# Optimization experiments

Hardware: AMD Instinct MI355X
Metric: run time of the kernel (lower is better)

Reference implementation:

```python
import jax, jax.numpy as jnp
import numpy as np

N = 20000      # nodes per graph
E = 640000     # edges per graph
FIN = 256      # input feature dim
H = 512        # hidden dim
K = 1000       # top_k


def _ln(x, g, b):
    m = jnp.mean(x, axis=-1, keepdims=True)
    v = jnp.var(x, axis=-1, keepdims=True)
    return (x - m) / jnp.sqrt(v + 1e-5) * g + b


def _gin_conv(x, src, dst, w1, b1, w2, b2):
    # GINConv with eps=0: mlp(x + sum_{j->i} x_j)
    agg = jax.ops.segment_sum(x[src], dst, num_segments=N)
    h = x + agg
    return jax.nn.relu(h @ w1 + b1) @ w2 + b2


def _gnn(x, edge_index, layers, lin_w, lin_b):
    src, dst = edge_index[0], edge_index[1]
    for (w1, b1, w2, b2) in layers:
        x = jax.nn.relu(_gin_conv(x, src, dst, w1, b1, w2, b2))
    return x @ lin_w + lin_b  # [N, 2]


def setup_inputs() -> dict:
    key = jax.random.key(0)
    ks = iter(jax.random.split(key, 40))
    w = lambda shape, s=0.02: jax.random.normal(next(ks), shape, jnp.float32) * s
    d = {}
    d["x1"] = jax.random.normal(next(ks), (N, FIN), jnp.float32)
    d["edge_index1"] = jax.random.randint(next(ks), (2, E), 0, N)
    d["x2"] = jax.random.normal(next(ks), (N, FIN), jnp.float32)
    d["edge_index2"] = jax.random.randint(next(ks), (2, E), 0, N)
    d["g_w11"] = w((FIN, H)); d["g_b11"] = jnp.zeros((H,), jnp.float32)
    d["g_w12"] = w((H, H));   d["g_b12"] = jnp.zeros((H,), jnp.float32)
    d["g_w21"] = w((H, H));   d["g_b21"] = jnp.zeros((H,), jnp.float32)
    d["g_w22"] = w((H, H));   d["g_b22"] = jnp.zeros((H,), jnp.float32)
    d["g_w31"] = w((H, H));   d["g_b31"] = jnp.zeros((H,), jnp.float32)
    d["g_w32"] = w((H, H));   d["g_b32"] = jnp.zeros((H,), jnp.float32)
    d["lin_w"] = w((H, 2));   d["lin_b"] = jnp.zeros((2,), jnp.float32)
    d["fc1_w"] = w((K, 128)); d["fc1_b"] = jnp.zeros((128,), jnp.float32)
    d["ln1_g"] = jnp.ones((128,), jnp.float32); d["ln1_b"] = jnp.zeros((128,), jnp.float32)
    d["fc2_w"] = w((128, H)); d["fc2_b"] = jnp.zeros((H,), jnp.float32)
    d["ln2_g"] = jnp.ones((H,), jnp.float32); d["ln2_b"] = jnp.zeros((H,), jnp.float32)
    d["fc3_w"] = w((H, 1));   d["fc3_b"] = jnp.zeros((1,), jnp.float32)
    return d


def reference(x1, edge_index1, x2, edge_index2,
              g_w11, g_b11, g_w12, g_b12,
              g_w21, g_b21, g_w22, g_b22,
              g_w31, g_b31, g_w32, g_b32,
              lin_w, lin_b,
              fc1_w, fc1_b, ln1_g, ln1_b,
              fc2_w, fc2_b, ln2_g, ln2_b,
              fc3_w, fc3_b):
    layers = [(g_w11, g_b11, g_w12, g_b12),
              (g_w21, g_b21, g_w22, g_b22),
              (g_w31, g_b31, g_w32, g_b32)]
    o1 = _gnn(x1, edge_index1, layers, lin_w, lin_b)  # [N, 2]
    o2 = _gnn(x2, edge_index2, layers, lin_w, lin_b)  # [N, 2]
    # torch.nn.PairwiseDistance(p=2, eps=1e-6): ||x1 - x2 + eps||_2 per row
    dist = jnp.sqrt(jnp.sum((o1 - o2 + 1e-6) ** 2, axis=-1))  # [N]
    vals, _ = jax.lax.top_k(dist, K)  # descending, matches torch.topk
    h = vals @ fc1_w + fc1_b
    h = jax.nn.relu(_ln(h, ln1_g, ln1_b))
    # dropout is identity in eval mode
    h = h @ fc2_w + fc2_b
    h = jax.nn.relu(_ln(h, ln2_g, ln2_b))
    return jax.nn.sigmoid(h @ fc3_w + fc3_b)  # [1]
```

## Files before the change

kernel.cpp:

```cpp
#include <hip/hip_runtime.h>
#include <hip/hip_bf16.h>
#include <math.h>

#define N1      20000
#define NT      40000
#define E1      640000
#define ET      1280000
#define FIN_D   256
#define HID_D   512
#define TOPK    1000
#define MP1     20096
#define NGEMM   628
#define AGG256  1250
#define AGG512  2500

#define NB       157
#define CAP      10240
#define BK_CHUNK 8192

typedef __attribute__((ext_vector_type(8))) short short8;
typedef __attribute__((ext_vector_type(4))) float floatx4;
typedef __attribute__((ext_vector_type(2))) float floatx2;
typedef unsigned int uintx4 __attribute__((ext_vector_type(4)));

__device__ __forceinline__ unsigned short f2bf(float f) {
    union { __hip_bfloat16 h; unsigned short u; } cv;
    cv.h = __float2bfloat16(f);
    return cv.u;
}
__device__ __forceinline__ float bflo(unsigned int u) {
    union { unsigned int i; float f; } c; c.i = u << 16; return c.f;
}
__device__ __forceinline__ float bfhi(unsigned int u) {
    union { unsigned int i; float f; } c; c.i = u & 0xffff0000u; return c.f;
}

__device__ __forceinline__ void gmap(int b, int& bx, int& by) {
    const int nfull = (157 / 8) * 32;
    if (b < nfull) {
        int chunk = b >> 5, w = b & 31;
        bx = (chunk << 3) + (w & 7);
        by = w >> 3;
    } else {
        int i = b - nfull;
        bx = 152 + i % 5;
        by = i / 5;
    }
}

__device__ __forceinline__ void convw_body(int bl, int K, float* tile ,
                                           const float* __restrict__ W,
                                           unsigned short* __restrict__ Wt) {
    int kb = K / 32;
    int k0 = (bl % kb) * 32, n0 = (bl / kb) * 32;
    int tx = threadIdx.x & 31, ty = threadIdx.x >> 5;
    for (int r = ty; r < 32; r += 8) tile[r * 33 + tx] = W[(size_t)(k0 + r) * HID_D + n0 + tx];
    __syncthreads();
    for (int r = ty; r < 32; r += 8)
        Wt[(size_t)(n0 + r) * K + k0 + tx] = f2bf(tile[tx * 33 + r]);
}
__device__ __forceinline__ void convx_body(int i, const float* __restrict__ x,
                                           unsigned char* __restrict__ x8) {
    float4 f = ((const float4*)x)[i];
    int p = __builtin_amdgcn_cvt_pk_fp8_f32(f.x, f.y, 0, false);
    p = __builtin_amdgcn_cvt_pk_fp8_f32(f.z, f.w, p, true);
    ((unsigned int*)x8)[i] = (unsigned int)p;
}

__device__ __forceinline__ void bucketA_body(int bb, int t,
                                             const int* __restrict__ ei1,
                                             const int* __restrict__ ei2,
                                             unsigned int* __restrict__ stageG,
                                             int* __restrict__ gcnt,
                                             unsigned int* shb) {
    unsigned int* stg   = shb;
    unsigned int* scn   = shb + 8192;
    unsigned int* hoff  = shb + 8448;
    unsigned int* hcur  = shb + 8608;
    unsigned int* hbase = shb + 8768;
    int e0 = bb * BK_CHUNK;
    int total = ET - e0; if (total > BK_CHUNK) total = BK_CHUNK;
    for (int i = t; i < 160; i += 256) hcur[i] = 0;
    __syncthreads();
    for (int k = 0; k < 32; ++k) {
        int e = e0 + k * 256 + t;
        if (e < ET) {
            int d = (e < E1) ? ei1[E1 + e] : (ei2[E1 + (e - E1)] + N1);
            atomicAdd(&hcur[d >> 8], 1u);
        }
    }
    __syncthreads();
    unsigned int v = (t < NB) ? hcur[t] : 0u;
    scn[t] = v; __syncthreads();
    for (int off = 1; off < 256; off <<= 1) {
        unsigned int x = (t >= off) ? scn[t - off] : 0u;
        __syncthreads(); scn[t] += x; __syncthreads();
    }
    if (t < NB) {
        unsigned int ex = scn[t] - v;
        hoff[t] = ex;
        hbase[t] = (unsigned int)atomicAdd(&gcnt[t], (int)v);
    }
    __syncthreads();
    if (t < NB) hcur[t] = hoff[t];
    __syncthreads();
    for (int k = 0; k < 32; ++k) {
        int e = e0 + k * 256 + t;
        if (e < ET) {
            int s, d;
            if (e < E1) { s = ei1[e]; d = ei1[E1 + e]; }
            else        { int ee = e - E1; s = ei2[ee] + N1; d = ei2[E1 + ee] + N1; }
            unsigned int b8 = (unsigned int)(d >> 8);
            unsigned int pos = atomicAdd(&hcur[b8], 1u);
            stg[pos] = (unsigned int)s | ((unsigned int)(d & 255) << 16) | (b8 << 24);
        }
    }
    __syncthreads();
    for (int i = t; i < total; i += 256) {
        unsigned int e = stg[i];
        unsigned int b8 = e >> 24;
        unsigned int g = hbase[b8] + ((unsigned int)i - hoff[b8]);
        if (g < CAP) stageG[(size_t)b8 * CAP + g] = e;
    }
}

__device__ __forceinline__ void sort_body(int b, int t,
                                          const unsigned int* __restrict__ stageG,
                                          const int* __restrict__ gcnt,
                                          int* __restrict__ row_start,
                                          unsigned short* __restrict__ csr,
                                          unsigned int* shb) {
    unsigned int* cnts = shb;
    unsigned int* offs = shb + 256;
    unsigned int* cur  = shb + 512;
    unsigned int* scn  = shb + 768;
    unsigned short* outb = (unsigned short*)(shb + 1024);
    int* s_base = (int*)(shb + 6144);
    unsigned int gv = (t < NB) ? (unsigned int)gcnt[t] : 0u;
    scn[t] = gv; __syncthreads();
    for (int off = 1; off < 256; off <<= 1) {
        unsigned int x = (t >= off) ? scn[t - off] : 0u;
        __syncthreads(); scn[t] += x; __syncthreads();
    }
    if (t == b) s_base[0] = (int)(scn[t] - gv);
    cnts[t] = 0;
    __syncthreads();
    int base = s_base[0];
    int cnt = gcnt[b]; if (cnt > CAP) cnt = CAP;
    const unsigned int* src = stageG + (size_t)b * CAP;
    for (int i = t; i < cnt; i += 256) atomicAdd(&cnts[(src[i] >> 16) & 255], 1u);
    __syncthreads();
    unsigned int v = cnts[t];
    offs[t] = v; __syncthreads();
    for (int off = 1; off < 256; off <<= 1) {
        unsigned int x = (t >= off) ? offs[t - off] : 0u;
        __syncthreads(); offs[t] += x; __syncthreads();
    }
    unsigned int excl = offs[t] - v;
    cur[t] = excl;
    int node = b * 256 + t;
    if (node < NT) row_start[node] = base + (int)excl;
    if (b == 0 && t == 0) row_start[NT] = ET;
    __syncthreads();
    for (int i = t; i < cnt; i += 256) {
        unsigned int e = src[i];
        unsigned int p = atomicAdd(&cur[(e >> 16) & 255], 1u);
        outb[p] = (unsigned short)(e & 0xffffu);
    }
    __syncthreads();
    for (int i = t; i < cnt; i += 256) csr[base + i] = outb[i];
}

#define ACC4(u) do { \
    acc2[0] += __builtin_amdgcn_cvt_pk_f32_fp8((int)(u).x, false); \
    acc2[1] += __builtin_amdgcn_cvt_pk_f32_fp8((int)(u).x, true);  \
    acc2[2] += __builtin_amdgcn_cvt_pk_f32_fp8((int)(u).y, false); \
    acc2[3] += __builtin_amdgcn_cvt_pk_f32_fp8((int)(u).y, true);  \
    acc2[4] += __builtin_amdgcn_cvt_pk_f32_fp8((int)(u).z, false); \
    acc2[5] += __builtin_amdgcn_cvt_pk_f32_fp8((int)(u).z, true);  \
    acc2[6] += __builtin_amdgcn_cvt_pk_f32_fp8((int)(u).w, false); \
    acc2[7] += __builtin_amdgcn_cvt_pk_f32_fp8((int)(u).w, true);  } while (0)

template<int LPR4, int NSLAB>
__device__ __forceinline__ void agg8_body(int ab, int tid,
                                          const unsigned char* __restrict__ x8,
                                          const int* __restrict__ row_start,
                                          const unsigned short* __restrict__ csr,
                                          unsigned short* __restrict__ h, int n0) {
    int slab = ab & (NSLAB - 1);
    int grp  = ab / NSLAB;
    int node = grp * 32 + (tid >> 3);
    int lanec = tid & 7;
    int chunk = slab * 8 + lanec;
    const uint4* Xc = (const uint4*)x8 + chunk;
    floatx2 acc2[8] = {};
    uint4 v = Xc[(size_t)node * LPR4];
    ACC4(v);
    int nid = n0 + node;
    int s = row_start[nid], e = row_start[nid + 1];
    int p = s;
    int nb = (e - s) >> 3;
    uint4 a0, a1, a2, a3, a4, a5, a6, a7;
    uint4 b0, b1, b2, b3, b4, b5, b6, b7;
#define LOAD8(R, P) do { \
    int q0 = (int)csr[(P) + 0] - n0, q1 = (int)csr[(P) + 1] - n0; \
    int q2 = (int)csr[(P) + 2] - n0, q3 = (int)csr[(P) + 3] - n0; \
    int q4 = (int)csr[(P) + 4] - n0, q5 = (int)csr[(P) + 5] - n0; \
    int q6 = (int)csr[(P) + 6] - n0, q7 = (int)csr[(P) + 7] - n0; \
    R##0 = Xc[(size_t)q0 * LPR4]; R##1 = Xc[(size_t)q1 * LPR4]; \
    R##2 = Xc[(size_t)q2 * LPR4]; R##3 = Xc[(size_t)q3 * LPR4]; \
    R##4 = Xc[(size_t)q4 * LPR4]; R##5 = Xc[(size_t)q5 * LPR4]; \
    R##6 = Xc[(size_t)q6 * LPR4]; R##7 = Xc[(size_t)q7 * LPR4]; } while (0)
#define ACC8(R) do { ACC4(R##0); ACC4(R##1); ACC4(R##2); ACC4(R##3); \
                     ACC4(R##4); ACC4(R##5); ACC4(R##6); ACC4(R##7); } while (0)
    if (nb > 0) {
        LOAD8(a, p); p += 8;
        int i = 1;
        for (; i + 1 < nb; i += 2) {
            LOAD8(b, p); p += 8;
            ACC8(a);
            LOAD8(a, p); p += 8;
            ACC8(b);
        }
        if (i < nb) { LOAD8(b, p); p += 8; ACC8(a); ACC8(b); }
        else        { ACC8(a); }
    }
#undef LOAD8
#undef ACC8
    for (; p + 2 <= e; p += 2) {
        int ma = (int)csr[p + 0] - n0, mb = (int)csr[p + 1] - n0;
        uint4 u0 = Xc[(size_t)ma * LPR4];
        uint4 u1 = Xc[(size_t)mb * LPR4];
        ACC4(u0); ACC4(u1);
    }
    if (p < e) {
        int ma = (int)csr[p] - n0;
        uint4 u0 = Xc[(size_t)ma * LPR4];
        ACC4(u0);
    }
    unsigned int ow[8];
#pragma unroll
    for (int i = 0; i < 8; ++i)
        ow[i] = (unsigned)f2bf(acc2[i].x) | ((unsigned)f2bf(acc2[i].y) << 16);
    uintx4 o0, o1;
    o0.x = ow[0]; o0.y = ow[1]; o0.z = ow[2]; o0.w = ow[3];
    o1.x = ow[4]; o1.y = ow[5]; o1.z = ow[6]; o1.w = ow[7];
    size_t base = ((size_t)node * LPR4 + chunk) * 2;
    ((uintx4*)h)[base + 0] = o0;
    ((uintx4*)h)[base + 1] = o1;
}

__launch_bounds__(256)
__global__ void prep1_kernel(const int* __restrict__ ei1, const int* __restrict__ ei2,
                             unsigned int* __restrict__ stageG, int* __restrict__ gcnt,
                             const float* __restrict__ x1, unsigned char* __restrict__ x8) {
    __shared__ unsigned int shb[8928];
    int b = blockIdx.x;
    if (b < NB) bucketA_body(b, threadIdx.x, ei1, ei2, stageG, gcnt, shb);
    else convx_body((b - NB) * 256 + threadIdx.x, x1, x8);
}

__launch_bounds__(256)
__global__ void fused_sortx(const unsigned int* __restrict__ stageG,
                            const int* __restrict__ gcnt,
                            int* __restrict__ row_start,
                            unsigned short* __restrict__ csr,
                            const float* __restrict__ x2,
                            unsigned char* __restrict__ x8g2) {
    __shared__ unsigned int shb[6152];
    int b = blockIdx.x;
    if (b < NB) sort_body(b, threadIdx.x, stageG, gcnt, row_start, csr, shb);
    else convx_body((b - NB) * 256 + threadIdx.x, x2, x8g2);
}

__launch_bounds__(256, 4)
__global__ void fused_aggw(const unsigned char* __restrict__ x8,
                           const int* __restrict__ row_start,
                           const unsigned short* __restrict__ csr,
                           unsigned short* __restrict__ h,
                           const float* w11, unsigned short* wt11,
                           const float* w12, unsigned short* wt12,
                           const float* w21, unsigned short* wt21,
                           const float* w22, unsigned short* wt22,
                           const float* w31, unsigned short* wt31,
                           const float* w32, unsigned short* wt32) {
    __shared__ float tile[32 * 33];
    int b = blockIdx.x;
    if (b < AGG256) {
        agg8_body<16, 2>(b, threadIdx.x, x8, row_start, csr, h, 0);
    } else {
        int bl = b - AGG256;
        if (bl < 128)       convw_body(bl,        FIN_D, tile, w11, wt11);
        else if (bl < 384)  convw_body(bl - 128,  HID_D, tile, w12, wt12);
        else if (bl < 640)  convw_body(bl - 384,  HID_D, tile, w21, wt21);
        else if (bl < 896)  convw_body(bl - 640,  HID_D, tile, w22, wt22);
        else if (bl < 1152) convw_body(bl - 896,  HID_D, tile, w31, wt31);
        else                convw_body(bl - 1152, HID_D, tile, w32, wt32);
    }
}

__device__ __forceinline__ void store_fp8_tile(int row0, int col0, int tid,
                                               unsigned short* smem,
                                               floatx4 acc[4][4], const float* __restrict__ bias,
                                               unsigned char* __restrict__ C8,
                                               int wr, int wc, int lane) {
    unsigned char* tile = (unsigned char*)smem;
    int q = lane >> 4, cn = lane & 15;
#pragma unroll
    for (int j = 0; j < 4; ++j) {
        int lcol = wc * 64 + j * 16 + cn;
        float bv = bias[col0 + lcol];
#pragma unroll
        for (int i = 0; i < 4; ++i) {
            int lrow = wr * 64 + i * 16 + q * 4;
#pragma unroll
            for (int r = 0; r < 4; ++r) {
                float vv = fmaxf(acc[i][j][r] + bv, 0.f);
                int t8 = __builtin_amdgcn_cvt_pk_fp8_f32(vv, 0.f, 0, false);
                tile[(lrow + r) * 128 + lcol] = (unsigned char)(t8 & 0xff);
            }
        }
    }
    __syncthreads();
#pragma unroll
    for (int it = 0; it < 4; ++it) {
        int idx = it * 256 + tid;
        int lrow = idx >> 3, c16 = idx & 7;
        *(uint4*)(C8 + (size_t)(row0 + lrow) * HID_D + col0 + c16 * 16) =
            *(const uint4*)(tile + lrow * 128 + c16 * 16);
    }
}

__device__ __forceinline__ void gemm_body_db(int bx, int by, int tid,
                                             unsigned short* smem,
                                             const unsigned short* __restrict__ A,
                                             const unsigned short* __restrict__ Wt,
                                             const float* __restrict__ bias,
                                             unsigned short* __restrict__ C,
                                             unsigned char* __restrict__ C8, int K) {
    const int N = HID_D;
    int lane = tid & 63;
    int w = tid >> 6;
    int wr = w >> 1, wc = w & 1;
    int row0 = bx * 128;
    int col0 = by * 128;
    floatx4 acc[4][4] = {};
    int lr = tid >> 2;
    int c8 = (tid & 3) * 8;
    const unsigned short* Ag = A + (size_t)row0 * K;
    const unsigned short* Bg = Wt + (size_t)col0 * K;
    int nt = K >> 5;
    {
        unsigned short* As = smem;
        unsigned short* Bs = smem + 4096;
#pragma unroll
        for (int l = 0; l < 2; ++l) {
            int r = l * 64 + lr;
            __builtin_amdgcn_global_load_lds(
                (const __attribute__((address_space(1))) void*)(Ag + (size_t)r * K + c8),
                (__attribute__((address_space(3))) void*)(As + l * 2048 + tid * 8),
                16, 0, 0);
            __builtin_amdgcn_global_load_lds(
                (const __attribute__((address_space(1))) void*)(Bg + (size_t)r * K + c8),
                (__attribute__((address_space(3))) void*)(Bs + l * 2048 + tid * 8),
                16, 0, 0);
        }
    }
    __syncthreads();
    for (int t = 0; t < nt; ++t) {
        unsigned short* As = smem + ((t & 1) ? 8192 : 0);
        unsigned short* Bs = As + 4096;
        if (t + 1 < nt) {
            unsigned short* An = smem + ((t & 1) ? 0 : 8192);
            unsigned short* Bn = An + 4096;
            int kt = (t + 1) << 5;
#pragma unroll
            for (int l = 0; l < 2; ++l) {
                int r = l * 64 + lr;
                __builtin_amdgcn_global_load_lds(
                    (const __attribute__((address_space(1))) void*)(Ag + (size_t)r * K + kt + c8),
                    (__attribute__((address_space(3))) void*)(An + l * 2048 + tid * 8),
                    16, 0, 0);
                __builtin_amdgcn_global_load_lds(
                    (const __attribute__((address_space(1))) void*)(Bg + (size_t)r * K + kt + c8),
                    (__attribute__((address_space(3))) void*)(Bn + l * 2048 + tid * 8),
                    16, 0, 0);
            }
        }
        short8 af[4], bf[4];
        int q8 = (lane >> 4) * 8;
#pragma unroll
        for (int i = 0; i < 4; ++i) {
            int m = wr * 64 + i * 16 + (lane & 15);
            af[i] = *(const short8*)&As[m * 32 + q8];
            int n = wc * 64 + i * 16 + (lane & 15);
            bf[i] = *(const short8*)&Bs[n * 32 + q8];
        }
#pragma unroll
        for (int i = 0; i < 4; ++i)
#pragma unroll
            for (int j = 0; j < 4; ++j)
                acc[i][j] = __builtin_amdgcn_mfma_f32_16x16x32_bf16(af[i], bf[j], acc[i][j], 0, 0, 0);
        __syncthreads();
    }
    if (C8) {
        store_fp8_tile(row0, col0, tid, smem, acc, bias, C8, wr, wc, lane);
        return;
    }
    int q = lane >> 4;
    int cn = lane & 15;
#pragma unroll
    for (int j = 0; j < 4; ++j) {
        int col = col0 + wc * 64 + j * 16 + cn;
        float bv = bias[col];
#pragma unroll
        for (int i = 0; i < 4; ++i) {
            int rowb = row0 + wr * 64 + i * 16 + q * 4;
#pragma unroll
            for (int r = 0; r < 4; ++r) {
                float vv = fmaxf(acc[i][j][r] + bv, 0.f);
                C[(size_t)(rowb + r) * N + col] = f2bf(vv);
            }
        }
    }
}

__launch_bounds__(256)
__global__ void gemm_pair(const unsigned short* __restrict__ A1,
                          const unsigned short* __restrict__ W1,
                          const float* __restrict__ b1,
                          unsigned short* __restrict__ C1, unsigned char* C81, int K1,
                          const unsigned short* __restrict__ A2,
                          const unsigned short* __restrict__ W2,
                          const float* __restrict__ b2,
                          unsigned short* __restrict__ C2, unsigned char* C82, int K2) {
    __shared__ unsigned short smem[16384];
    int b = blockIdx.x;
    int bx, by;
    if (b < NGEMM) {
        gmap(b, bx, by);
        gemm_body_db(bx, by, threadIdx.x, smem, A1, W1, b1, C1, C81, K1);
    } else {
        gmap(b - NGEMM, bx, by);
        gemm_body_db(bx, by, threadIdx.x, smem, A2, W2, b2, C2, C82, K2);
    }
}

template<int LPR4, int NSLAB>
__launch_bounds__(256)
__global__ void fused_k(const unsigned short* __restrict__ A,
                        const unsigned short* __restrict__ Wt,
                        const float* __restrict__ bias,
                        unsigned short* __restrict__ C, unsigned char* C8, int K,
                        const unsigned char* __restrict__ x8,
                        const int* __restrict__ row_start,
                        const unsigned short* __restrict__ csr,
                        unsigned short* __restrict__ h, int n0, int nGemm) {
    __shared__ unsigned short smem[16384];
    int b = blockIdx.x;
    if (b < nGemm) {
        int bx, by;
        gmap(b, bx, by);
        gemm_body_db(bx, by, threadIdx.x, smem, A, Wt, bias, C, C8, K);
    } else {
        agg8_body<LPR4, NSLAB>(b - nGemm, threadIdx.x, x8, row_start, csr, h, n0);
    }
}

__device__ __forceinline__ void lin_body(int bb, int tid, const unsigned short* __restrict__ A,
                                         const float* __restrict__ w, const float* __restrict__ b,
                                         float* __restrict__ o, int M) {
    int wave = tid >> 6;
    int lane = tid & 63;
    int row = bb * 4 + wave;
    if (row >= M) return;
    const uint4* Ar = (const uint4*)(A + (size_t)row * 512);
    uint4 u = Ar[lane];
    float f[8];
    f[0] = bflo(u.x); f[1] = bfhi(u.x); f[2] = bflo(u.y); f[3] = bfhi(u.y);
    f[4] = bflo(u.z); f[5] = bfhi(u.z); f[6] = bflo(u.w); f[7] = bfhi(u.w);
    float s0 = 0.f, s1 = 0.f;
#pragma unroll
    for (int j = 0; j < 8; ++j) {
        int base = (lane * 8 + j) * 2;
        s0 = fmaf(f[j], w[base + 0], s0);
        s1 = fmaf(f[j], w[base + 1], s1);
    }
#pragma unroll
    for (int off = 32; off > 0; off >>= 1) {
        s0 += __shfl_down(s0, off, 64);
        s1 += __shfl_down(s1, off, 64);
    }
    if (lane == 0) { o[row * 2] = s0 + b[0]; o[row * 2 + 1] = s1 + b[1]; }
}

__launch_bounds__(256)
__global__ void fused_gemmlin(const unsigned short* __restrict__ A,
                              const unsigned short* __restrict__ Wt,
                              const float* __restrict__ bias,
                              unsigned short* __restrict__ C, int K,
                              const unsigned short* __restrict__ L,
                              const float* __restrict__ lw, const float* __restrict__ lb,
                              float* __restrict__ o) {
    __shared__ unsigned short smem[16384];
    int b = blockIdx.x;
    if (b < NGEMM) {
        int bx, by;
        gmap(b, bx, by);
        gemm_body_db(bx, by, threadIdx.x, smem, A, Wt, bias, C, nullptr, K);
    } else {
        lin_body(b - NGEMM, threadIdx.x, L, lw, lb, o, N1);
    }
}

__global__ void lin_dist_kernel(const unsigned short* __restrict__ A,
                                const float* __restrict__ w, const float* __restrict__ b,
                                const float* __restrict__ o1,
                                float* __restrict__ o2out,
                                float* __restrict__ dist) {
    int tid = threadIdx.x;
    int wave = tid >> 6;
    int lane = tid & 63;
    int row = blockIdx.x * 4 + wave;
    if (row >= N1) return;
    const uint4* Ar = (const uint4*)(A + (size_t)row * 512);
    uint4 u = Ar[lane];
    float f[8];
    f[0] = bflo(u.x); f[1] = bfhi(u.x); f[2] = bflo(u.y); f[3] = bfhi(u.y);
    f[4] = bflo(u.z); f[5] = bfhi(u.z); f[6] = bflo(u.w); f[7] = bfhi(u.w);
    float s0 = 0.f, s1 = 0.f;
#pragma unroll
    for (int j = 0; j < 8; ++j) {
        int base = (lane * 8 + j) * 2;
        s0 = fmaf(f[j], w[base + 0], s0);
        s1 = fmaf(f[j], w[base + 1], s1);
    }
#pragma unroll
    for (int off = 32; off > 0; off >>= 1) {
        s0 += __shfl_down(s0, off, 64);
        s1 += __shfl_down(s1, off, 64);
    }
    if (lane == 0) {
        float vx = s0 + b[0], vy = s1 + b[1];
        o2out[row * 2] = vx; o2out[row * 2 + 1] = vy;
        float2 a = ((const float2*)o1)[row];
        float d0 = a.x - vx + 1e-6f, d1 = a.y - vy + 1e-6f;
        dist[row] = sqrtf(d0 * d0 + d1 * d1);
    }
}

#define HBLK 20
#define HPB  1000
__launch_bounds__(256)
__global__ void hist_lds_kernel(const float* __restrict__ dist, int* __restrict__ hist) {
    __shared__ int lh[4096];
    int t = threadIdx.x;
    for (int i = t; i < 4096; i += 256) lh[i] = 0;
    __syncthreads();
    int base = blockIdx.x * HPB;
    for (int i = t; i < HPB; i += 256) {
        int idx = base + i;
        if (idx < N1) atomicAdd(&lh[__float_as_uint(dist[idx]) >> 19], 1);
    }
    __syncthreads();
    for (int i = t; i < 4096; i += 256) {
        int v = lh[i];
        if (v) atomicAdd(&hist[i], v);
    }
}

__global__ void selk_kernel(const int* __restrict__ hist, int* __restrict__ selout) {
    __shared__ int tile[256];
    int t = threadIdx.x;
    int running = 0;
    for (int tb = 0; tb < 16; ++tb) {
        int idx = 4095 - (tb * 256 + t);
        int v = hist[idx];
        tile[t] = v;
        __syncthreads();
        for (int off = 1; off < 256; off <<= 1) {
            int x = (t >= off) ? tile[t - off] : 0;
            __syncthreads();
            tile[t] += x;
            __syncthreads();
        }
        int incl = running + tile[t];
        if (incl >= TOPK && incl - v < TOPK) selout[0] = idx;
        running += tile[255];
        __syncthreads();
        if (running >= TOPK) break;
    }
}

__global__ void compact_kernel(const float* __restrict__ dist, const int* __restrict__ selout,
                               int* __restrict__ nc, float* __restrict__ cd, int* __restrict__ ci) {
    int i = blockIdx.x * blockDim.x + threadIdx.x;
    if (i >= N1) return;
    float d = dist[i];
    int b = (int)(__float_as_uint(d) >> 19);
    if (b >= selout[0]) {
        int p = atomicAdd(nc, 1);
        cd[p] = d;
        ci[p] = i;
    }
}

#define CCH 2048
__global__ void rankc_kernel(const float* __restrict__ cd, const int* __restrict__ ci,
                             const int* __restrict__ nc_p, float* __restrict__ vals) {
    __shared__ float ds[CCH];
    __shared__ int   di_[CCH];
    int nc = *nc_p;
    if (blockIdx.x * 256 >= nc) return;
    int t = threadIdx.x;
    int q = blockIdx.x * 256 + t;
    float dq = 0.f; int iq = 0;
    if (q < nc) { dq = cd[q]; iq = ci[q]; }
    int cnt = 0;
    for (int c0 = 0; c0 < nc; c0 += CCH) {
        int lim = min(CCH, nc - c0);
        for (int j = t; j < lim; j += 256) { ds[j] = cd[c0 + j]; di_[j] = ci[c0 + j]; }
        __syncthreads();
        if (q < nc) {
            for (int j = 0; j < lim; ++j) {
                float dj = ds[j];
                cnt += (dj > dq) || (dj == dq && di_[j] < iq);
            }
        }
        __syncthreads();
    }
    if (q < nc && cnt < TOPK) vals[cnt] = dq;
}

__launch_bounds__(512)
__global__ void head_kernel(const float* __restrict__ vals,
                            const float* __restrict__ fc1_w, const float* __restrict__ fc1_b,
                            const float* __restrict__ ln1_g, const float* __restrict__ ln1_b,
                            const float* __restrict__ fc2_w, const float* __restrict__ fc2_b,
                            const float* __restrict__ ln2_g, const float* __restrict__ ln2_b,
                            const float* __restrict__ fc3_w, const float* __restrict__ fc3_b,
                            float* __restrict__ out) {
    __shared__ float sv[TOPK];
    __shared__ float a1[128];
    __shared__ float red[512];
    __shared__ float s_m, s_r;
    int t = threadIdx.x;
    for (int i = t; i < TOPK; i += 512) sv[i] = vals[i];
    __syncthreads();
    int g = t >> 7, c = t & 127;
    float part = 0.f;
    for (int j = g * 250; j < g * 250 + 250; ++j)
        part = fmaf(sv[j], fc1_w[j * 128 + c], part);
    red[t] = part;
    __syncthreads();
    float h1 = 0.f;
    if (t < 128) h1 = fc1_b[t] + red[t] + red[t + 128] + red[t + 256] + red[t + 384];
    __syncthreads();
    red[t] = (t < 128) ? h1 : 0.f; __syncthreads();
    for (int s = 256; s > 0; s >>= 1) { if (t < s) red[t] += red[t + s]; __syncthreads(); }
    if (t == 0) s_m = red[0] / 128.f;
    __syncthreads();
    float m1 = s_m;
    float dv = (t < 128) ? (h1 - m1) : 0.f;
    red[t] = dv * dv; __syncthreads();
    for (int s = 256; s > 0; s >>= 1) { if (t < s) red[t] += red[t + s]; __syncthreads(); }
    if (t == 0) s_r = rsqrtf(red[0] / 128.f + 1e-5f);
    __syncthreads();
    float r1 = s_r;
    if (t < 128) a1[t] = fmaxf((h1 - m1) * r1 * ln1_g[t] + ln1_b[t], 0.f);
    __syncthreads();
    float h2 = fc2_b[t];
    for (int j = 0; j < 128; ++j) h2 = fmaf(a1[j], fc2_w[j * 512 + t], h2);
    red[t] = h2; __syncthreads();
    for (int s = 256; s > 0; s >>= 1) { if (t < s) red[t] += red[t + s]; __syncthreads(); }
    if (t == 0) s_m = red[0] / 512.f;
    __syncthreads();
    float m2 = s_m;
    float d2 = h2 - m2;
    red[t] = d2 * d2; __syncthreads();
    for (int s = 256; s > 0; s >>= 1) { if (t < s) red[t] += red[t + s]; __syncthreads(); }
    if (t == 0) s_r = rsqrtf(red[0] / 512.f + 1e-5f);
    __syncthreads();
    float r2 = s_r;
    float y2 = fmaxf((h2 - m2) * r2 * ln2_g[t] + ln2_b[t], 0.f);
    red[t] = y2 * fc3_w[t]; __syncthreads();
    for (int s = 256; s > 0; s >>= 1) { if (t < s) red[t] += red[t + s]; __syncthreads(); }
    if (t == 0) out[0] = 1.f / (1.f + expf(-(red[0] + fc3_b[0])));
}

extern "C" void kernel_launch(void* const* d_in, const int* in_sizes, int n_in,
                              void* d_out, int out_size, void* d_ws, size_t ws_size,
                              hipStream_t stream) {
    const float* x1   = (const float*)d_in[0];
    const int*   ei1  = (const int*)d_in[1];
    const float* x2   = (const float*)d_in[2];
    const int*   ei2  = (const int*)d_in[3];
    const float* w11  = (const float*)d_in[4];
    const float* b11  = (const float*)d_in[5];
    const float* w12  = (const float*)d_in[6];
    const float* b12  = (const float*)d_in[7];
    const float* w21  = (const float*)d_in[8];
    const float* b21  = (const float*)d_in[9];
    const float* w22  = (const float*)d_in[10];
    const float* b22  = (const float*)d_in[11];
    const float* w31  = (const float*)d_in[12];
    const float* b31  = (const float*)d_in[13];
    const float* w32  = (const float*)d_in[14];
    const float* b32  = (const float*)d_in[15];
    const float* lw   = (const float*)d_in[16];
    const float* lb   = (const float*)d_in[17];
    const float* fc1w = (const float*)d_in[18];
    const float* fc1b = (const float*)d_in[19];
    const float* ln1g = (const float*)d_in[20];
    const float* ln1b = (const float*)d_in[21];
    const float* fc2w = (const float*)d_in[22];
    const float* fc2b = (const float*)d_in[23];
    const float* ln2g = (const float*)d_in[24];
    const float* ln2b = (const float*)d_in[25];
    const float* fc3w = (const float*)d_in[26];
    const float* fc3b = (const float*)d_in[27];

    char* ws = (char*)d_ws;
    size_t off = 0;
    auto alloc = [&](size_t bytes) -> void* {
        void* p = ws + off;
        off += (bytes + 255) & ~(size_t)255;
        return p;
    };
    unsigned char*  XB8 = (unsigned char*)alloc((size_t)NT * FIN_D);
    unsigned short* H0a = (unsigned short*)alloc((size_t)MP1 * HID_D * 2);
    unsigned short* H1a = (unsigned short*)alloc((size_t)MP1 * HID_D * 2);
    unsigned short* H0b = (unsigned short*)alloc((size_t)MP1 * HID_D * 2);
    unsigned short* H1b = (unsigned short*)alloc((size_t)MP1 * HID_D * 2);
    unsigned char*  F8a = (unsigned char*)alloc((size_t)MP1 * HID_D);
    unsigned char*  F8b = (unsigned char*)alloc((size_t)MP1 * HID_D);
    unsigned short* wt11 = (unsigned short*)alloc((size_t)HID_D * FIN_D * 2);
    unsigned short* wt12 = (unsigned short*)alloc((size_t)HID_D * HID_D * 2);
    unsigned short* wt21 = (unsigned short*)alloc((size_t)HID_D * HID_D * 2);
    unsigned short* wt22 = (unsigned short*)alloc((size_t)HID_D * HID_D * 2);
    unsigned short* wt31 = (unsigned short*)alloc((size_t)HID_D * HID_D * 2);
    unsigned short* wt32 = (unsigned short*)alloc((size_t)HID_D * HID_D * 2);
    float* o         = (float*)alloc((size_t)NT * 2 * 4);
    float* dist      = (float*)alloc((size_t)N1 * 4);
    float* vals      = (float*)alloc((size_t)TOPK * 4);
    int*   row_start = (int*)alloc((size_t)(NT + 1) * 4);
    unsigned short* csr16 = (unsigned short*)alloc((size_t)ET * 2);
    unsigned int* stageG  = (unsigned int*)alloc((size_t)NB * CAP * 4);
    int*   gcnt      = (int*)alloc((size_t)160 * 4);
    int*   selblk    = (int*)alloc((size_t)(4096 + 64) * 4);
    int*   hist      = selblk;
    int*   nc        = selblk + 4096;
    int*   selout    = (int*)alloc(2 * 4);
    float* cd        = (float*)alloc((size_t)N1 * 4);
    int*   ci        = (int*)alloc((size_t)N1 * 4);

    const unsigned char* XB8g2 = XB8 + (size_t)N1 * FIN_D;

    hipMemsetAsync(gcnt, 0, 160 * sizeof(int), stream);
    hipMemsetAsync(selblk, 0, (4096 + 64) * sizeof(int), stream);
    prep1_kernel<<<NB + 5000, 256, 0, stream>>>(ei1, ei2, stageG, gcnt, x1, XB8);
    fused_sortx<<<NB + 5000, 256, 0, stream>>>(stageG, gcnt, row_start, csr16,
                                               x2, (unsigned char*)XB8g2);
    fused_aggw<<<AGG256 + 1408, 256, 0, stream>>>(
        XB8, row_start, csr16, H0a,
        w11, wt11, w12, wt12, w21, wt21, w22, wt22, w31, wt31, w32, wt32);

    fused_k<16, 2><<<NGEMM + AGG256, 256, 0, stream>>>(H0a, wt11, b11, H1a, nullptr, FIN_D,
                                                       XB8g2, row_start, csr16, H0b, N1, NGEMM);
    gemm_pair<<<2 * NGEMM, 256, 0, stream>>>(H1a, wt12, b12, nullptr, F8a, HID_D,
                                             H0b, wt11, b11, H1b, nullptr, FIN_D);
    fused_k<32, 4><<<NGEMM + AGG512, 256, 0, stream>>>(H1b, wt12, b12, nullptr, F8b, HID_D,
                                                       F8a, row_start, csr16, H1a, 0, NGEMM);
    fused_k<32, 4><<<NGEMM + AGG512, 256, 0, stream>>>(H1a, wt21, b21, H0a, nullptr, HID_D,
                                                       F8b, row_start, csr16, H1b, N1, NGEMM);
    gemm_pair<<<2 * NGEMM, 256, 0, stream>>>(H0a, wt22, b22, nullptr, F8a, HID_D,
                                             H1b, wt21, b21, H0b, nullptr, HID_D);
    fused_k<32, 4><<<NGEMM + AGG512, 256, 0, stream>>>(H0b, wt22, b22, nullptr, F8b, HID_D,
                                                       F8a, row_start, csr16, H1a, 0, NGEMM);
    fused_k<32, 4><<<NGEMM + AGG512, 256, 0, stream>>>(H1a, wt31, b31, H0a, nullptr, HID_D,
                                                       F8b, row_start, csr16, H1b, N1, NGEMM);
    gemm_pair<<<2 * NGEMM, 256, 0, stream>>>(H0a, wt32, b32, H1a, nullptr, HID_D,
                                             H1b, wt31, b31, H0b, nullptr, HID_D);
    fused_gemmlin<<<NGEMM + (N1 + 3) / 4, 256, 0, stream>>>(H0b, wt32, b32, H1b, HID_D,
                                                            H1a, lw, lb, o);
    lin_dist_kernel<<<(N1 + 3) / 4, 256, 0, stream>>>(H1b, lw, lb, o,
                                                      o + 2 * (size_t)N1, dist);
    hist_lds_kernel<<<HBLK, 256, 0, stream>>>(dist, hist);

    selk_kernel<<<1, 256, 0, stream>>>(hist, selout);
    compact_kernel<<<(N1 + 255) / 256, 256, 0, stream>>>(dist, selout, nc, cd, ci);
    rankc_kernel<<<(N1 + 255) / 256, 256, 0, stream>>>(cd, ci, nc, vals);
    head_kernel<<<1, 512, 0, stream>>>(vals, fc1w, fc1b, ln1g, ln1b,
                                       fc2w, fc2b, ln2g, ln2b, fc3w, fc3b,
                                       (float*)d_out);
}
```

Before: 670.1 us.

## Triple-buffer LDS staging in GEMM bodies with one barrier per k-step

Adds a triple-buffered GEMM body that prefetches two k-tiles ahead via direct global-to-LDS loads. It uses partial vmcnt waits and a single barrier per iteration, replacing the double-buffered version in gemm_pair and fused_gemmlin. The aim is to hide global load latency and halve barrier count per k-step. It raises shared memory per block from 32KB to 48KB, which may reduce occupancy, and the fused_k path still uses the old body.

```diff
diff --git a/kernel.cpp b/kernel.cpp
--- a/kernel.cpp
+++ b/kernel.cpp
@@ -331,6 +331,27 @@
     }
 }
 
+__device__ __forceinline__ void store_bf16(int row0, int col0, int wr, int wc, int lane,
+                                           floatx4 acc[4][4], const float* __restrict__ bias,
+                                           unsigned short* __restrict__ C) {
+    int q = lane >> 4;
+    int cn = lane & 15;
+#pragma unroll
+    for (int j = 0; j < 4; ++j) {
+        int col = col0 + wc * 64 + j * 16 + cn;
+        float bv = bias[col];
+#pragma unroll
+        for (int i = 0; i < 4; ++i) {
+            int rowb = row0 + wr * 64 + i * 16 + q * 4;
+#pragma unroll
+            for (int r = 0; r < 4; ++r) {
+                float vv = fmaxf(acc[i][j][r] + bv, 0.f);
+                C[(size_t)(rowb + r) * HID_D + col] = f2bf(vv);
+            }
+        }
+    }
+}
+
 __device__ __forceinline__ void gemm_body_db(int bx, int by, int tid,
                                              unsigned short* smem,
                                              const unsigned short* __restrict__ A,
@@ -338,7 +359,6 @@
                                              const float* __restrict__ bias,
                                              unsigned short* __restrict__ C,
                                              unsigned char* __restrict__ C8, int K) {
-    const int N = HID_D;
     int lane = tid & 63;
     int w = tid >> 6;
     int wr = w >> 1, wc = w & 1;
@@ -407,22 +427,74 @@
         store_fp8_tile(row0, col0, tid, smem, acc, bias, C8, wr, wc, lane);
         return;
     }
-    int q = lane >> 4;
-    int cn = lane & 15;
-#pragma unroll
-    for (int j = 0; j < 4; ++j) {
-        int col = col0 + wc * 64 + j * 16 + cn;
-        float bv = bias[col];
+    store_bf16(row0, col0, wr, wc, lane, acc, bias, C);
+}
+
+__device__ __forceinline__ void gemm_body_tb(int bx, int by, int tid,
+                                             unsigned short* smem ,
+                                             const unsigned short* __restrict__ A,
+                                             const unsigned short* __restrict__ Wt,
+                                             const float* __restrict__ bias,
+                                             unsigned short* __restrict__ C,
+                                             unsigned char* __restrict__ C8, int K) {
+    int lane = tid & 63;
+    int w = tid >> 6;
+    int wr = w >> 1, wc = w & 1;
+    int row0 = bx * 128;
+    int col0 = by * 128;
+    floatx4 acc[4][4] = {};
+    int lr = tid >> 2;
+    int c8 = (tid & 3) * 8;
+    const unsigned short* Ag = A + (size_t)row0 * K;
+    const unsigned short* Bg = Wt + (size_t)col0 * K;
+    int nt = K >> 5;
+#define STAGE_TB(TI, SLOT) do { \
+    unsigned short* As_ = smem + (SLOT) * 8192; \
+    unsigned short* Bs_ = As_ + 4096; \
+    int kt_ = (TI) << 5; \
+    _Pragma("unroll") \
+    for (int l = 0; l < 2; ++l) { \
+        int r = l * 64 + lr; \
+        __builtin_amdgcn_global_load_lds( \
+            (const __attribute__((address_space(1))) void*)(Ag + (size_t)r * K + kt_ + c8), \
+            (__attribute__((address_space(3))) void*)(As_ + l * 2048 + tid * 8), 16, 0, 0); \
+        __builtin_amdgcn_global_load_lds( \
+            (const __attribute__((address_space(1))) void*)(Bg + (size_t)r * K + kt_ + c8), \
+            (__attribute__((address_space(3))) void*)(Bs_ + l * 2048 + tid * 8), 16, 0, 0); \
+    } } while (0)
+    STAGE_TB(0, 0);
+    if (nt > 1) STAGE_TB(1, 1);
+    for (int t = 0; t < nt; ++t) {
+        if (t + 1 < nt) { asm volatile("s_waitcnt vmcnt(4)" ::: "memory"); }
+        else            { asm volatile("s_waitcnt vmcnt(0)" ::: "memory"); }
+        __builtin_amdgcn_sched_barrier(0);
+        __builtin_amdgcn_s_barrier();
+        __builtin_amdgcn_sched_barrier(0);
+        if (t + 2 < nt) STAGE_TB(t + 2, (t + 2) % 3);
+        unsigned short* As = smem + (t % 3) * 8192;
+        unsigned short* Bs = As + 4096;
+        short8 af[4], bf[4];
+        int q8 = (lane >> 4) * 8;
 #pragma unroll
         for (int i = 0; i < 4; ++i) {
-            int rowb = row0 + wr * 64 + i * 16 + q * 4;
-#pragma unroll
-            for (int r = 0; r < 4; ++r) {
-                float vv = fmaxf(acc[i][j][r] + bv, 0.f);
-                C[(size_t)(rowb + r) * N + col] = f2bf(vv);
-            }
-        }
-    }
+            int m = wr * 64 + i * 16 + (lane & 15);
+            af[i] = *(const short8*)&As[m * 32 + q8];
+            int n = wc * 64 + i * 16 + (lane & 15);
+            bf[i] = *(const short8*)&Bs[n * 32 + q8];
+        }
+#pragma unroll
+        for (int i = 0; i < 4; ++i)
+#pragma unroll
+            for (int j = 0; j < 4; ++j)
+                acc[i][j] = __builtin_amdgcn_mfma_f32_16x16x32_bf16(af[i], bf[j], acc[i][j], 0, 0, 0);
+    }
+#undef STAGE_TB
+    __syncthreads();
+    if (C8) {
+        store_fp8_tile(row0, col0, tid, smem, acc, bias, C8, wr, wc, lane);
+        return;
+    }
+    store_bf16(row0, col0, wr, wc, lane, acc, bias, C);
 }
 
 __launch_bounds__(256)
@@ -434,15 +506,15 @@
                           const unsigned short* __restrict__ W2,
                           const float* __restrict__ b2,
                           unsigned short* __restrict__ C2, unsigned char* C82, int K2) {
-    __shared__ unsigned short smem[16384];
+    __shared__ unsigned short smem[24576];
     int b = blockIdx.x;
     int bx, by;
     if (b < NGEMM) {
         gmap(b, bx, by);
-        gemm_body_db(bx, by, threadIdx.x, smem, A1, W1, b1, C1, C81, K1);
+        gemm_body_tb(bx, by, threadIdx.x, smem, A1, W1, b1, C1, C81, K1);
     } else {
         gmap(b - NGEMM, bx, by);
-        gemm_body_db(bx, by, threadIdx.x, smem, A2, W2, b2, C2, C82, K2);
+        gemm_body_tb(bx, by, threadIdx.x, smem, A2, W2, b2, C2, C82, K2);
     }
 }
 
@@ -502,12 +574,12 @@
                               const unsigned short* __restrict__ L,
                               const float* __restrict__ lw, const float* __restrict__ lb,
                               float* __restrict__ o) {
-    __shared__ unsigned short smem[16384];
+    __shared__ unsigned short smem[24576];
     int b = blockIdx.x;
     if (b < NGEMM) {
         int bx, by;
         gmap(b, bx, by);
-        gemm_body_db(bx, by, threadIdx.x, smem, A, Wt, bias, C, nullptr, K);
+        gemm_body_tb(bx, by, threadIdx.x, smem, A, Wt, bias, C, nullptr, K);
     } else {
         lin_body(b - NGEMM, threadIdx.x, L, lw, lb, o, N1);
     }
```

Result: slower. 683.7 us (+2.0%).

## Triple-buffer GEMM LDS tiles with explicit vmcnt waits and one barrier per step

Applied to the files above, without the earlier changes.

Replaces the double-buffered async global-to-LDS GEMM pipeline with a three-slot ring that prefetches two k-tiles ahead. Each step waits only for the older outstanding loads via s_waitcnt vmcnt and uses a single barrier instead of two. The aim is to hide more global latency and cut barrier overhead in the MFMA loop. It raises shared memory per block from 32KB to 48KB, which may lower occupancy for GEMM and the co-scheduled aggregation blocks.

```diff
diff --git a/kernel.cpp b/kernel.cpp
--- a/kernel.cpp
+++ b/kernel.cpp
@@ -331,14 +331,13 @@
     }
 }
 
-__device__ __forceinline__ void gemm_body_db(int bx, int by, int tid,
-                                             unsigned short* smem,
+__device__ __forceinline__ void gemm_body_tb(int bx, int by, int tid,
+                                             unsigned short* smem ,
                                              const unsigned short* __restrict__ A,
                                              const unsigned short* __restrict__ Wt,
                                              const float* __restrict__ bias,
                                              unsigned short* __restrict__ C,
                                              unsigned char* __restrict__ C8, int K) {
-    const int N = HID_D;
     int lane = tid & 63;
     int w = tid >> 6;
     int wr = w >> 1, wc = w & 1;
@@ -350,43 +349,31 @@
     const unsigned short* Ag = A + (size_t)row0 * K;
     const unsigned short* Bg = Wt + (size_t)col0 * K;
     int nt = K >> 5;
-    {
-        unsigned short* As = smem;
-        unsigned short* Bs = smem + 4096;
-#pragma unroll
-        for (int l = 0; l < 2; ++l) {
-            int r = l * 64 + lr;
-            __builtin_amdgcn_global_load_lds(
-                (const __attribute__((address_space(1))) void*)(Ag + (size_t)r * K + c8),
-                (__attribute__((address_space(3))) void*)(As + l * 2048 + tid * 8),
-                16, 0, 0);
-            __builtin_amdgcn_global_load_lds(
-                (const __attribute__((address_space(1))) void*)(Bg + (size_t)r * K + c8),
-                (__attribute__((address_space(3))) void*)(Bs + l * 2048 + tid * 8),
-                16, 0, 0);
-        }
-    }
-    __syncthreads();
+#define STAGE_TB(TI, SLOT) do { \
+    unsigned short* As_ = smem + (SLOT) * 8192; \
+    unsigned short* Bs_ = As_ + 4096; \
+    int kt_ = (TI) << 5; \
+    _Pragma("unroll") \
+    for (int l = 0; l < 2; ++l) { \
+        int r = l * 64 + lr; \
+        __builtin_amdgcn_global_load_lds( \
+            (const __attribute__((address_space(1))) void*)(Ag + (size_t)r * K + kt_ + c8), \
+            (__attribute__((address_space(3))) void*)(As_ + l * 2048 + tid * 8), 16, 0, 0); \
+        __builtin_amdgcn_global_load_lds( \
+            (const __attribute__((address_space(1))) void*)(Bg + (size_t)r * K + kt_ + c8), \
+            (__attribute__((address_space(3))) void*)(Bs_ + l * 2048 + tid * 8), 16, 0, 0); \
+    } } while (0)
+    STAGE_TB(0, 0);
+    if (nt > 1) STAGE_TB(1, 1);
     for (int t = 0; t < nt; ++t) {
-        unsigned short* As = smem + ((t & 1) ? 8192 : 0);
+        if (t + 1 < nt) { asm volatile("s_waitcnt vmcnt(4)" ::: "memory"); }
+        else            { asm volatile("s_waitcnt vmcnt(0)" ::: "memory"); }
+        __builtin_amdgcn_sched_barrier(0);
+        __builtin_amdgcn_s_barrier();
+        __builtin_amdgcn_sched_barrier(0);
+        if (t + 2 < nt) STAGE_TB(t + 2, (t + 2) % 3);
+        unsigned short* As = smem + (t % 3) * 8192;
         unsigned short* Bs = As + 4096;
-        if (t + 1 < nt) {
-            unsigned short* An = smem + ((t & 1) ? 0 : 8192);
-            unsigned short* Bn = An + 4096;
-            int kt = (t + 1) << 5;
-#pragma unroll
-            for (int l = 0; l < 2; ++l) {
-                int r = l * 64 + lr;
-                __builtin_amdgcn_global_load_lds(
-                    (const __attribute__((address_space(1))) void*)(Ag + (size_t)r * K + kt + c8),
-                    (__attribute__((address_space(3))) void*)(An + l * 2048 + tid * 8),
-                    16, 0, 0);
-                __builtin_amdgcn_global_load_lds(
-                    (const __attribute__((address_space(1))) void*)(Bg + (size_t)r * K + kt + c8),
-                    (__attribute__((address_space(3))) void*)(Bn + l * 2048 + tid * 8),
-                    16, 0, 0);
-            }
-        }
         short8 af[4], bf[4];
         int q8 = (lane >> 4) * 8;
 #pragma unroll
@@ -401,8 +388,9 @@
 #pragma unroll
             for (int j = 0; j < 4; ++j)
                 acc[i][j] = __builtin_amdgcn_mfma_f32_16x16x32_bf16(af[i], bf[j], acc[i][j], 0, 0, 0);
-        __syncthreads();
-    }
+    }
+#undef STAGE_TB
+    __syncthreads();
     if (C8) {
         store_fp8_tile(row0, col0, tid, smem, acc, bias, C8, wr, wc, lane);
         return;
@@ -419,7 +407,7 @@
 #pragma unroll
             for (int r = 0; r < 4; ++r) {
                 float vv = fmaxf(acc[i][j][r] + bv, 0.f);
-                C[(size_t)(rowb + r) * N + col] = f2bf(vv);
+                C[(size_t)(rowb + r) * HID_D + col] = f2bf(vv);
             }
         }
     }
@@ -434,15 +422,15 @@
                           const unsigned short* __restrict__ W2,
                           const float* __restrict__ b2,
                           unsigned short* __restrict__ C2, unsigned char* C82, int K2) {
-    __shared__ unsigned short smem[16384];
+    __shared__ unsigned short smem[24576];
     int b = blockIdx.x;
     int bx, by;
     if (b < NGEMM) {
         gmap(b, bx, by);
-        gemm_body_db(bx, by, threadIdx.x, smem, A1, W1, b1, C1, C81, K1);
+        gemm_body_tb(bx, by, threadIdx.x, smem, A1, W1, b1, C1, C81, K1);
     } else {
         gmap(b - NGEMM, bx, by);
-        gemm_body_db(bx, by, threadIdx.x, smem, A2, W2, b2, C2, C82, K2);
+        gemm_body_tb(bx, by, threadIdx.x, smem, A2, W2, b2, C2, C82, K2);
     }
 }
 
@@ -456,12 +444,12 @@
                         const int* __restrict__ row_start,
                         const unsigned short* __restrict__ csr,
                         unsigned short* __restrict__ h, int n0, int nGemm) {
-    __shared__ unsigned short smem[16384];
+    __shared__ unsigned short smem[24576];
     int b = blockIdx.x;
     if (b < nGemm) {
         int bx, by;
         gmap(b, bx, by);
-        gemm_body_db(bx, by, threadIdx.x, smem, A, Wt, bias, C, C8, K);
+        gemm_body_tb(bx, by, threadIdx.x, smem, A, Wt, bias, C, C8, K);
     } else {
         agg8_body<LPR4, NSLAB>(b - nGemm, threadIdx.x, x8, row_start, csr, h, n0);
     }
@@ -502,12 +490,12 @@
                               const unsigned short* __restrict__ L,
                               const float* __restrict__ lw, const float* __restrict__ lb,
                               float* __restrict__ o) {
-    __shared__ unsigned short smem[16384];
+    __shared__ unsigned short smem[24576];
     int b = blockIdx.x;
     if (b < NGEMM) {
         int bx, by;
         gmap(b, bx, by);
-        gemm_body_db(bx, by, threadIdx.x, smem, A, Wt, bias, C, nullptr, K);
+        gemm_body_tb(bx, by, threadIdx.x, smem, A, Wt, bias, C, nullptr, K);
     } else {
         lin_body(b - NGEMM, threadIdx.x, L, lw, lb, o, N1);
     }
```

Result: slower. 685.4 us (+2.3%).
